# Kernel optimization log

Measured on AMD Instinct MI355X. Metric: run time of the kernel, lower is better.

Reference implementation:

```python
import jax, jax.numpy as jnp
import numpy as np

NU, NF, E, FIN, H = 50000, 25000, 500000, 128, 128
NEG_SLOPE_ATT = 0.2   # PyG GATConv default negative_slope
NEG_SLOPE_MLP = 0.01  # nn.LeakyReLU default
BN_EPS = 1e-5


def setup_inputs() -> dict:
    key = jax.random.key(0)
    ks = iter(jax.random.split(key, 64))

    def rn(shape, scale=0.05):
        return jax.random.normal(next(ks), shape, dtype=jnp.float32) * scale

    inp = {
        "x_user": jax.random.normal(next(ks), (NU, FIN), dtype=jnp.float32),
        "x_food": jax.random.normal(next(ks), (NF, FIN), dtype=jnp.float32),
        "uf_src": jax.random.randint(next(ks), (E,), 0, NU),
        "uf_dst": jax.random.randint(next(ks), (E,), 0, NF),
        "fu_src": jax.random.randint(next(ks), (E,), 0, NF),
        "fu_dst": jax.random.randint(next(ks), (E,), 0, NU),
        "he_user": jax.random.randint(next(ks), (E,), 0, NU),
        "he_food": jax.random.randint(next(ks), (E,), 0, NF),
        "batch_health_scores": jax.random.uniform(next(ks), (E,), dtype=jnp.float32),
    }
    # GATConv params per layer (1,2) per edge type (uf: user->food, fu: food->user)
    for L, fin in ((1, FIN), (2, H)):
        for et in ("uf", "fu"):
            inp[f"w{L}_{et}_src"] = rn((fin, H))
            inp[f"w{L}_{et}_dst"] = rn((fin, H))
            inp[f"a{L}_{et}_src"] = rn((H,))
            inp[f"a{L}_{et}_dst"] = rn((H,))
            inp[f"b{L}_{et}"] = jnp.zeros((H,), jnp.float32)
    # BatchNorm per layer per node type
    for L in (1, 2):
        for nt in ("user", "food"):
            inp[f"bn{L}_{nt}_g"] = jnp.ones((H,), jnp.float32)
            inp[f"bn{L}_{nt}_b"] = jnp.zeros((H,), jnp.float32)
    # health preference MLP: Linear(H, H//2) -> LeakyReLU -> Linear(H//2, 1) -> Tanh
    inp["hw1"] = rn((H, H // 2)); inp["hb1"] = jnp.zeros((H // 2,), jnp.float32)
    inp["hw2"] = rn((H // 2, 1)); inp["hb2"] = jnp.zeros((1,), jnp.float32)
    return inp


def _gat(x_src, x_dst, src, dst, w_s, w_d, a_s, a_d, b, n_dst):
    """PyG GATConv, heads=1, no self loops, eval (no attention dropout)."""
    hs = x_src @ w_s                      # [Ns, H]
    hd = x_dst @ w_d                      # [Nd, H]
    asn = hs @ a_s                        # per-src-node scalar
    adn = hd @ a_d                        # per-dst-node scalar
    e = jax.nn.leaky_relu(asn[src] + adn[dst], NEG_SLOPE_ATT)  # [E]
    m = jax.ops.segment_max(e, dst, num_segments=n_dst)
    m = jnp.where(jnp.isfinite(m), m, 0.0)
    ee = jnp.exp(e - m[dst])
    den = jax.ops.segment_sum(ee, dst, num_segments=n_dst)
    alpha = ee / (den[dst] + 1e-16)
    out = jax.ops.segment_sum(alpha[:, None] * hs[src], dst, num_segments=n_dst)
    return out + b


def _bn_elu(x, g, b):
    mu = x.mean(0)
    var = x.var(0)  # biased var, as torch BN uses for normalization
    return jax.nn.elu((x - mu) * jax.lax.rsqrt(var + BN_EPS) * g + b)


def reference(x_user, x_food, uf_src, uf_dst, fu_src, fu_dst, he_user, he_food,
              batch_health_scores,
              w1_uf_src, w1_uf_dst, a1_uf_src, a1_uf_dst, b1_uf,
              w1_fu_src, w1_fu_dst, a1_fu_src, a1_fu_dst, b1_fu,
              w2_uf_src, w2_uf_dst, a2_uf_src, a2_uf_dst, b2_uf,
              w2_fu_src, w2_fu_dst, a2_fu_src, a2_fu_dst, b2_fu,
              bn1_user_g, bn1_user_b, bn1_food_g, bn1_food_b,
              bn2_user_g, bn2_user_b, bn2_food_g, bn2_food_b,
              hw1, hb1, hw2, hb2):
    # ---- layer 1 (HeteroConv, sum aggr; each node type has one incoming edge type)
    xf = _gat(x_user, x_food, uf_src, uf_dst, w1_uf_src, w1_uf_dst, a1_uf_src, a1_uf_dst, b1_uf, NF)
    xu = _gat(x_food, x_user, fu_src, fu_dst, w1_fu_src, w1_fu_dst, a1_fu_src, a1_fu_dst, b1_fu, NU)
    xu = _bn_elu(xu, bn1_user_g, bn1_user_b)
    xf = _bn_elu(xf, bn1_food_g, bn1_food_b)
    # ---- layer 2
    xf2 = _gat(xu, xf, uf_src, uf_dst, w2_uf_src, w2_uf_dst, a2_uf_src, a2_uf_dst, b2_uf, NF)
    xu2 = _gat(xf, xu, fu_src, fu_dst, w2_fu_src, w2_fu_dst, a2_fu_src, a2_fu_dst, b2_fu, NU)
    xu2 = _bn_elu(xu2, bn2_user_g, bn2_user_b)
    xf2 = _bn_elu(xf2, bn2_food_g, bn2_food_b)
    # ---- health-score scatter_add update
    h = jax.nn.leaky_relu(xu2 @ hw1 + hb1, NEG_SLOPE_MLP)
    prefs = jnp.tanh(h @ hw2 + hb2)                      # [NU, 1]
    adjusted = prefs[he_user, 0] * batch_health_scores   # [E]
    # expand+scatter_add over rows == broadcast segment_sum of the per-edge scalar
    s = jax.ops.segment_sum(adjusted, he_food, num_segments=NF)  # [NF]
    xf2 = xf2 + 0.1 * s[:, None]
    return (xu2, xf2, prefs)
```

## Files before the change

kernel.cpp:

```cpp
#include <hip/hip_runtime.h>
#include <cstddef>

#define NU_ 50000
#define NF_ 25000
#define E_  500000
#define CAPF_ 96
#define CAPU_ 48

typedef __attribute__((ext_vector_type(8))) short short8v;
typedef __attribute__((ext_vector_type(4))) float float4v;

constexpr int LDR = 136;

static __device__ __forceinline__ ushort f2bf(float f) {
    uint u = __float_as_uint(f);
    uint r = (u + 0x7fffu + ((u >> 16) & 1u)) >> 16;
    return (ushort)r;
}
static __device__ __forceinline__ float bf2f(ushort u) {
    return __uint_as_float(((uint)u) << 16);
}

struct PPArgs {
    const int* uf_src; const int* uf_dst;
    const int* fu_src; const int* fu_dst;
    int* deg_f; int* deg_u;
    ushort* buck_f; ushort* buck_u;
    const float* xu; const float* xf;
    ushort* bu; ushort* bfo;
    const float* W[5];  ushort* T[5];
    const float* waW[8]; const float* waA[8];
    float* vall;
};

__global__ __launch_bounds__(256) void preprocess(PPArgs A) {
    const int EB  = (E_ + 255) / 256;
    const int nbA = NU_ * 32 / 256;
    const int nbB = NF_ * 32 / 256;
    const int nbC = 4 * 64 + 32;
    int b = blockIdx.x, t = threadIdx.x;
    if (b < 2 * EB) {
        const int *src, *dst; int *deg; ushort* buck; int cap, e;
        if (b < EB) { src = A.uf_src; dst = A.uf_dst; deg = A.deg_f; buck = A.buck_f; cap = CAPF_; e = b * 256 + t; }
        else        { src = A.fu_src; dst = A.fu_dst; deg = A.deg_u; buck = A.buck_u; cap = CAPU_; e = (b - EB) * 256 + t; }
        if (e < E_) {
            int d = dst[e];
            int r = atomicAdd(&deg[d], 1);
            if (r < cap) buck[d * cap + r] = (ushort)src[e];
        }
        return;
    }
    b -= 2 * EB;
    if (b < nbA) {
        int i = b * 256 + t;
        float4 v = ((const float4*)A.xu)[i];
        ushort4 o; o.x = f2bf(v.x); o.y = f2bf(v.y); o.z = f2bf(v.z); o.w = f2bf(v.w);
        ((ushort4*)A.bu)[i] = o;
    } else if (b < nbA + nbB) {
        int i = (b - nbA) * 256 + t;
        float4 v = ((const float4*)A.xf)[i];
        ushort4 o; o.x = f2bf(v.x); o.y = f2bf(v.y); o.z = f2bf(v.z); o.w = f2bf(v.w);
        ((ushort4*)A.bfo)[i] = o;
    } else if (b < nbA + nbB + nbC) {
        int cb = b - nbA - nbB;
        int m, wb, sh;
        if (cb < 256) { m = cb >> 6; wb = cb & 63; sh = 7; }
        else          { m = 4; wb = cb - 256; sh = 6; }
        int idx = wb * 256 + t;
        int k = idx >> sh, c = idx & ((1 << sh) - 1);
        A.T[m][c * 128 + k] = f2bf(A.W[m][idx]);
    } else {
        int db = b - nbA - nbB - nbC;
        int row = db * 4 + (t >> 6);
        int m = row >> 7, k = row & 127, lane = t & 63;
        float2 w = ((const float2*)(A.waW[m] + k * 128))[lane];
        float2 av = ((const float2*)A.waA[m])[lane];
        float s = w.x * av.x + w.y * av.y;
        #pragma unroll
        for (int o = 32; o; o >>= 1) s += __shfl_xor(s, o);
        if (lane == 0) A.vall[row] = s;
    }
}

static __device__ __forceinline__ void gemm_tile(const ushort* __restrict__ Xb,
                                                 const ushort* __restrict__ Wt,
                                                 ushort* __restrict__ C, int N, int row0,
                                                 const float* __restrict__ va, const float* __restrict__ vb,
                                                 float* __restrict__ oa, float* __restrict__ ob,
                                                 short* Xs, short* Ws) {
    const int t = threadIdx.x;
    for (int i = t; i < 128 * 16; i += 256) {
        int r = i >> 4, c8 = (i & 15) << 3;
        short8v v = {};
        if (row0 + r < N) v = *(const short8v*)(Xb + (size_t)(row0 + r) * 128 + c8);
        *(short8v*)(&Xs[r * LDR + c8]) = v;
    }
    for (int i = t; i < 128 * 16; i += 256) {
        int r = i >> 4, c8 = (i & 15) << 3;
        *(short8v*)(&Ws[r * LDR + c8]) = *(const short8v*)(Wt + r * 128 + c8);
    }
    __syncthreads();

    const int w = t >> 6, l = t & 63;
    const int m0 = (w & 1) * 64;
    const int n0 = (w >> 1) * 64;
    const int frow = l & 15;
    const int koff = (l >> 4) << 3;

    float4v acc[4][4];
    #pragma unroll
    for (int m = 0; m < 4; ++m)
        #pragma unroll
        for (int n = 0; n < 4; ++n) acc[m][n] = (float4v)0.f;

    #pragma unroll
    for (int ks = 0; ks < 4; ++ks) {
        const int k0 = ks * 32 + koff;
        short8v a[4], b[4];
        #pragma unroll
        for (int m = 0; m < 4; ++m)
            a[m] = *(const short8v*)(&Xs[(m0 + m * 16 + frow) * LDR + k0]);
        #pragma unroll
        for (int n = 0; n < 4; ++n)
            b[n] = *(const short8v*)(&Ws[(n0 + n * 16 + frow) * LDR + k0]);
        #pragma unroll
        for (int m = 0; m < 4; ++m)
            #pragma unroll
            for (int n = 0; n < 4; ++n)
                acc[m][n] = __builtin_amdgcn_mfma_f32_16x16x32_bf16(a[m], b[n], acc[m][n], 0, 0, 0);
    }

    const int crow = (l >> 4) << 2;
    const int ccol = l & 15;
    #pragma unroll
    for (int m = 0; m < 4; ++m) {
        #pragma unroll
        for (int r4 = 0; r4 < 4; ++r4) {
            int grow = row0 + m0 + m * 16 + crow + r4;
            if (grow < N) {
                #pragma unroll
                for (int n = 0; n < 4; ++n)
                    C[(size_t)grow * 128 + n0 + n * 16 + ccol] = f2bf(acc[m][n][r4]);
            }
        }
    }

    float2 va2 = ((const float2*)va)[l];
    float2 vb2 = ((const float2*)vb)[l];
    for (int rr = 0; rr < 32; ++rr) {
        int r = w * 32 + rr;
        ushort2 xv = *(const ushort2*)(&Xs[r * LDR + l * 2]);
        float fx = bf2f(xv.x), fy = bf2f(xv.y);
        float s1 = fx * va2.x + fy * va2.y;
        float s2 = fx * vb2.x + fy * vb2.y;
        #pragma unroll
        for (int o = 32; o; o >>= 1) { s1 += __shfl_xor(s1, o); s2 += __shfl_xor(s2, o); }
        int grow = row0 + r;
        if (l == 0 && grow < N) { oa[grow] = s1; ob[grow] = s2; }
    }
}

__global__ __launch_bounds__(256) void gemm_both(
        const ushort* __restrict__ Xu, const ushort* __restrict__ Wtu, ushort* __restrict__ Cu,
        const float* __restrict__ vau, const float* __restrict__ vbu,
        float* __restrict__ oau, float* __restrict__ obu,
        const ushort* __restrict__ Xf, const ushort* __restrict__ Wtf, ushort* __restrict__ Cf,
        const float* __restrict__ vaf, const float* __restrict__ vbf,
        float* __restrict__ oaf, float* __restrict__ obf) {
    __shared__ short Xs[128 * LDR];
    __shared__ short Ws[128 * LDR];
    const int GU = (NU_ + 127) / 128;
    if ((int)blockIdx.x < GU)
        gemm_tile(Xu, Wtu, Cu, NU_, blockIdx.x * 128, vau, vbu, oau, obu, Xs, Ws);
    else
        gemm_tile(Xf, Wtf, Cf, NF_, (blockIdx.x - GU) * 128, vaf, vbf, oaf, obf, Xs, Ws);
}

__global__ __launch_bounds__(256) void gat_agg_both(
        const int* __restrict__ deg_f, const ushort* __restrict__ buck_f,
        const float* __restrict__ asn_u, const float* __restrict__ adn_f,
        const ushort* __restrict__ hs_u, ushort* __restrict__ out_f,
        const int* __restrict__ deg_u, const ushort* __restrict__ buck_u,
        const float* __restrict__ asn_f, const float* __restrict__ adn_u,
        const ushort* __restrict__ hs_f, ushort* __restrict__ out_u) {
    const int NBAF = (NF_ + 3) / 4;
    int blk = blockIdx.x;
    const int* deg; const ushort* buck; const float *asn, *adn; const ushort* hs; ushort* out; int Nd, d, cap;
    if (blk < NBAF) {
        deg = deg_f; buck = buck_f; asn = asn_u; adn = adn_f; hs = hs_u; out = out_f;
        Nd = NF_; cap = CAPF_; d = blk * 4 + (threadIdx.x >> 6);
    } else {
        deg = deg_u; buck = buck_u; asn = asn_f; adn = adn_u; hs = hs_f; out = out_u;
        Nd = NU_; cap = CAPU_; d = (blk - NBAF) * 4 + (threadIdx.x >> 6);
    }
    int lane = threadIdx.x & 63;
    if (d >= Nd) return;
    const int beg = d * cap;
    const int end = beg + min(deg[d], cap);
    const float ad = adn[d];
    const int qw = lane >> 4, l16 = lane & 15;
    float acc[8] = {0.f, 0.f, 0.f, 0.f, 0.f, 0.f, 0.f, 0.f};
    float den = 0.f;
    for (int base = beg; base < end; base += 64) {
        int e = base + lane;
        int s = 0; float ev = 0.f;
        if (e < end) {
            s = buck[e];
            float v = asn[s] + ad;
            v = v > 0.f ? v : 0.2f * v;
            ev = __expf(v);
        }
        float r = ev;
        #pragma unroll
        for (int o = 32; o; o >>= 1) r += __shfl_xor(r, o);
        den += r;
        int cnt4 = (min(64, end - base) + 3) & ~3;
        for (int j = 0; j < cnt4; j += 8) {
            int jj = j + qw;
            float ev0 = __shfl(ev, jj);
            int   sj0 = __shfl(s, jj);
            short8v h0 = *(const short8v*)(hs + (size_t)sj0 * 128 + l16 * 8);
            if (j + 4 < cnt4) {
                float ev1 = __shfl(ev, jj + 4);
                int   sj1 = __shfl(s, jj + 4);
                short8v h1 = *(const short8v*)(hs + (size_t)sj1 * 128 + l16 * 8);
                #pragma unroll
                for (int k = 0; k < 8; ++k)
                    acc[k] += ev0 * bf2f((ushort)h0[k]) + ev1 * bf2f((ushort)h1[k]);
            } else {
                #pragma unroll
                for (int k = 0; k < 8; ++k)
                    acc[k] += ev0 * bf2f((ushort)h0[k]);
            }
        }
    }
    #pragma unroll
    for (int k = 0; k < 8; ++k) {
        acc[k] += __shfl_xor(acc[k], 16);
        acc[k] += __shfl_xor(acc[k], 32);
    }
    if (qw == 0) {
        float inv = 1.f / (den + 1e-16f);
        short8v o;
        #pragma unroll
        for (int k = 0; k < 8; ++k) o[k] = (short)f2bf(acc[k] * inv);
        *(short8v*)(out + (size_t)d * 128 + l16 * 8) = o;
    }
}

__global__ __launch_bounds__(256) void bn_stats2b(const ushort* __restrict__ x1, float* __restrict__ stat1,
                                                  int N1, int B1,
                                                  const ushort* __restrict__ x2, float* __restrict__ stat2,
                                                  int N2, int B2) {
    const ushort* x; float* stat; int N, b, nb;
    if ((int)blockIdx.x < B1) { x = x1; stat = stat1; N = N1; b = blockIdx.x; nb = B1; }
    else { x = x2; stat = stat2; N = N2; b = blockIdx.x - B1; nb = B2; }
    const int t = threadIdx.x;
    const int rg = t >> 4;
    const int c16 = t & 15;
    float s[8] = {0,0,0,0,0,0,0,0}, q[8] = {0,0,0,0,0,0,0,0};
    for (int r = b * 16 + rg; r < N; r += nb * 16) {
        short8v v = *(const short8v*)(x + (size_t)r * 128 + c16 * 8);
        #pragma unroll
        for (int k = 0; k < 8; ++k) {
            float f = bf2f((ushort)v[k]);
            s[k] += f; q[k] += f * f;
        }
    }
    #pragma unroll
    for (int k = 0; k < 8; ++k) {
        s[k] += __shfl_xor(s[k], 16); q[k] += __shfl_xor(q[k], 16);
        s[k] += __shfl_xor(s[k], 32); q[k] += __shfl_xor(q[k], 32);
    }
    __shared__ float rs[4][128], rq[4][128];
    const int w = t >> 6, l = t & 63;
    if (l < 16) {
        #pragma unroll
        for (int k = 0; k < 8; ++k) {
            rs[w][l * 8 + k] = s[k];
            rq[w][l * 8 + k] = q[k];
        }
    }
    __syncthreads();
    if (t < 128) {
        atomicAdd(&stat[t],       rs[0][t] + rs[1][t] + rs[2][t] + rs[3][t]);
        atomicAdd(&stat[128 + t], rq[0][t] + rq[1][t] + rq[2][t] + rq[3][t]);
    }
}

static __device__ __forceinline__ void bn_scale_shift(const float* __restrict__ stat,
                                                      const float* __restrict__ g,
                                                      const float* __restrict__ b,
                                                      float invN, int c0,
                                                      float* sc, float* sh) {
    #pragma unroll
    for (int k = 0; k < 8; ++k) {
        int c = c0 + k;
        float mu  = stat[c] * invN;
        float var = stat[128 + c] * invN - mu * mu;
        float s = g[c] * rsqrtf(var + 1e-5f);
        sc[k] = s;
        sh[k] = b[c] - mu * s;
    }
}

__global__ void bn_apply2b(const ushort* __restrict__ x1, const float* __restrict__ stat1,
                           const float* __restrict__ g1, const float* __restrict__ b1, float invN1,
                           float* __restrict__ xo1, ushort* __restrict__ xb1, int N1,
                           const ushort* __restrict__ x2, const float* __restrict__ stat2,
                           const float* __restrict__ g2, const float* __restrict__ b2, float invN2,
                           float* __restrict__ xo2, ushort* __restrict__ xb2, int N2) {
    int i = blockIdx.x * 256 + threadIdx.x;
    const ushort* x; const float *stat, *g, *b; float invN; float* xo; ushort* xb;
    if (i < N1 * 16) { x = x1; stat = stat1; g = g1; b = b1; invN = invN1; xo = xo1; xb = xb1; }
    else {
        i -= N1 * 16;
        if (i >= N2 * 16) return;
        x = x2; stat = stat2; g = g2; b = b2; invN = invN2; xo = xo2; xb = xb2;
    }
    int c16 = i & 15;
    short8v v = *(const short8v*)(x + (size_t)i * 8);
    float sc[8], sh[8];
    bn_scale_shift(stat, g, b, invN, c16 * 8, sc, sh);
    float o[8];
    #pragma unroll
    for (int k = 0; k < 8; ++k) {
        float f = bf2f((ushort)v[k]) * sc[k] + sh[k];
        o[k] = f > 0.f ? f : __expf(f) - 1.f;
    }
    if (xo) {
        *(float4*)(xo + (size_t)i * 8)     = make_float4(o[0], o[1], o[2], o[3]);
        *(float4*)(xo + (size_t)i * 8 + 4) = make_float4(o[4], o[5], o[6], o[7]);
    }
    if (xb) {
        short8v u;
        #pragma unroll
        for (int k = 0; k < 8; ++k) u[k] = (short)f2bf(o[k]);
        *(short8v*)(xb + (size_t)i * 8) = u;
    }
}

__global__ void bn_apply1b(const ushort* __restrict__ x, const float* __restrict__ stat,
                           const float* __restrict__ g, const float* __restrict__ b, float invN,
                           float* __restrict__ xo, ushort* __restrict__ xb, int N,
                           const float* __restrict__ health) {
    int i = blockIdx.x * 256 + threadIdx.x;
    if (i >= N * 16) return;
    int c16 = i & 15;
    short8v v = *(const short8v*)(x + (size_t)i * 8);
    float sc[8], sh[8];
    bn_scale_shift(stat, g, b, invN, c16 * 8, sc, sh);
    float hv = health ? 0.1f * health[i >> 4] : 0.f;
    float o[8];
    #pragma unroll
    for (int k = 0; k < 8; ++k) {
        float f = bf2f((ushort)v[k]) * sc[k] + sh[k];
        o[k] = (f > 0.f ? f : __expf(f) - 1.f) + hv;
    }
    if (xo) {
        *(float4*)(xo + (size_t)i * 8)     = make_float4(o[0], o[1], o[2], o[3]);
        *(float4*)(xo + (size_t)i * 8 + 4) = make_float4(o[4], o[5], o[6], o[7]);
    }
    if (xb) {
        short8v u;
        #pragma unroll
        for (int k = 0; k < 8; ++k) u[k] = (short)f2bf(o[k]);
        *(short8v*)(xb + (size_t)i * 8) = u;
    }
}

__global__ __launch_bounds__(256) void mlp_mfma(const ushort* __restrict__ Xb,
                                                const ushort* __restrict__ Wt,
                                                const float* __restrict__ hb1,
                                                const float* __restrict__ hw2,
                                                const float* __restrict__ hb2,
                                                float* __restrict__ prefs, int N) {
    __shared__ short Xs[128 * LDR];
    __shared__ short Ws[64 * LDR];
    const int t = threadIdx.x;
    const int row0 = blockIdx.x * 128;

    for (int i = t; i < 128 * 16; i += 256) {
        int r = i >> 4, c8 = (i & 15) << 3;
        short8v v = {};
        if (row0 + r < N) v = *(const short8v*)(Xb + (size_t)(row0 + r) * 128 + c8);
        *(short8v*)(&Xs[r * LDR + c8]) = v;
    }
    for (int i = t; i < 64 * 16; i += 256) {
        int r = i >> 4, c8 = (i & 15) << 3;
        *(short8v*)(&Ws[r * LDR + c8]) = *(const short8v*)(Wt + r * 128 + c8);
    }
    __syncthreads();

    const int w = t >> 6, l = t & 63;
    const int m0 = w * 32;
    const int frow = l & 15;
    const int koff = (l >> 4) << 3;

    float4v acc[2][4];
    #pragma unroll
    for (int m = 0; m < 2; ++m)
        #pragma unroll
        for (int n = 0; n < 4; ++n) acc[m][n] = (float4v)0.f;

    #pragma unroll
    for (int ks = 0; ks < 4; ++ks) {
        const int k0 = ks * 32 + koff;
        short8v a[2], b[4];
        #pragma unroll
        for (int m = 0; m < 2; ++m)
            a[m] = *(const short8v*)(&Xs[(m0 + m * 16 + frow) * LDR + k0]);
        #pragma unroll
        for (int n = 0; n < 4; ++n)
            b[n] = *(const short8v*)(&Ws[(n * 16 + frow) * LDR + k0]);
        #pragma unroll
        for (int m = 0; m < 2; ++m)
            #pragma unroll
            for (int n = 0; n < 4; ++n)
                acc[m][n] = __builtin_amdgcn_mfma_f32_16x16x32_bf16(a[m], b[n], acc[m][n], 0, 0, 0);
    }

    float hb1v[4], hw2v[4];
    #pragma unroll
    for (int n = 0; n < 4; ++n) {
        int col = n * 16 + (l & 15);
        hb1v[n] = hb1[col];
        hw2v[n] = hw2[col];
    }
    const float hb2v = hb2[0];
    #pragma unroll
    for (int m = 0; m < 2; ++m) {
        #pragma unroll
        for (int r4 = 0; r4 < 4; ++r4) {
            float p = 0.f;
            #pragma unroll
            for (int n = 0; n < 4; ++n) {
                float v = acc[m][n][r4] + hb1v[n];
                v = v > 0.f ? v : 0.01f * v;
                p += v * hw2v[n];
            }
            p += __shfl_xor(p, 1);
            p += __shfl_xor(p, 2);
            p += __shfl_xor(p, 4);
            p += __shfl_xor(p, 8);
            int grow = row0 + m0 + m * 16 + ((l >> 4) << 2) + r4;
            if ((l & 15) == 0 && grow < N) prefs[grow] = tanhf(p + hb2v);
        }
    }
}

__global__ void health_scatter(const int* __restrict__ hu, const int* __restrict__ hf,
                               const float* __restrict__ score, const float* __restrict__ prefs,
                               float* __restrict__ s, int E) {
    int e = blockIdx.x * 256 + threadIdx.x;
    if (e >= E) return;
    atomicAdd(&s[hf[e]], prefs[hu[e]] * score[e]);
}

extern "C" void kernel_launch(void* const* d_in, const int* in_sizes, int n_in,
                              void* d_out, int out_size, void* d_ws, size_t ws_size,
                              hipStream_t stream) {
    const float* x_user = (const float*)d_in[0];
    const float* x_food = (const float*)d_in[1];
    const int* uf_src = (const int*)d_in[2];
    const int* uf_dst = (const int*)d_in[3];
    const int* fu_src = (const int*)d_in[4];
    const int* fu_dst = (const int*)d_in[5];
    const int* he_user = (const int*)d_in[6];
    const int* he_food = (const int*)d_in[7];
    const float* scores = (const float*)d_in[8];
    const float* bn1_user_g = (const float*)d_in[29];
    const float* bn1_user_b = (const float*)d_in[30];
    const float* bn1_food_g = (const float*)d_in[31];
    const float* bn1_food_b = (const float*)d_in[32];
    const float* bn2_user_g = (const float*)d_in[33];
    const float* bn2_user_b = (const float*)d_in[34];
    const float* bn2_food_g = (const float*)d_in[35];
    const float* bn2_food_b = (const float*)d_in[36];
    const float* hw1 = (const float*)d_in[37];
    const float* hb1 = (const float*)d_in[38];
    const float* hw2 = (const float*)d_in[39];
    const float* hb2 = (const float*)d_in[40];

    float* outp  = (float*)d_out;
    float* xu2   = outp;
    float* xf2   = outp + (size_t)NU_ * 128;
    float* prefs = xf2 + (size_t)NF_ * 128;

    float* ws = (float*)d_ws;
    ushort* hs_u = (ushort*)ws;
    ushort* hs_f = hs_u + (size_t)NU_ * 128;
    float* base1 = ws + (size_t)(NU_ + NF_) * 64;
    ushort* xu1b = (ushort*)base1;
    ushort* xf1b = xu1b + (size_t)NU_ * 128;
    float* base2 = base1 + (size_t)(NU_ + NF_) * 64;
    ushort* xu2b = (ushort*)base2;
    ushort* xf2b = xu2b + (size_t)NU_ * 128;
    float* base3 = base2 + (size_t)(NU_ + NF_) * 64;
    float* asn_u = base3;
    float* adn_u = asn_u + NU_;
    float* asn_f = adn_u + NU_;
    float* adn_f = asn_f + NF_;
    float* stat4 = adn_f + NF_;
    float* sbuf  = stat4 + 1024;
    int*   deg_f = (int*)(sbuf + NF_);
    int*   deg_u = deg_f + NF_;
    ushort* buck_f = (ushort*)(deg_u + NU_);
    ushort* buck_u = buck_f + (size_t)NF_ * CAPF_;
    ushort* wt0  = buck_u + (size_t)NU_ * CAPU_;
    ushort* wt1  = wt0 + 16384;
    ushort* wt2  = wt1 + 16384;
    ushort* wt3  = wt2 + 16384;
    ushort* hw1t = wt3 + 16384;
    float* vall  = (float*)(hw1t + 8192);

    const size_t zero_elems = 1024 + NF_ + NF_ + NU_;
    hipMemsetAsync(stat4, 0, zero_elems * sizeof(float), stream);

    const int EB = (E_ + 255) / 256;
    PPArgs pp;
    pp.uf_src = uf_src; pp.uf_dst = uf_dst;
    pp.fu_src = fu_src; pp.fu_dst = fu_dst;
    pp.deg_f = deg_f; pp.deg_u = deg_u;
    pp.buck_f = buck_f; pp.buck_u = buck_u;
    pp.xu = x_user; pp.xf = x_food; pp.bu = xu2b; pp.bfo = xf2b;
    pp.W[0] = (const float*)d_in[9];  pp.T[0] = wt0;
    pp.W[1] = (const float*)d_in[14]; pp.T[1] = wt1;
    pp.W[2] = (const float*)d_in[19]; pp.T[2] = wt2;
    pp.W[3] = (const float*)d_in[24]; pp.T[3] = wt3;
    pp.W[4] = hw1;                    pp.T[4] = hw1t;
    pp.waW[0] = (const float*)d_in[9];  pp.waA[0] = (const float*)d_in[11];
    pp.waW[1] = (const float*)d_in[10]; pp.waA[1] = (const float*)d_in[12];
    pp.waW[2] = (const float*)d_in[14]; pp.waA[2] = (const float*)d_in[16];
    pp.waW[3] = (const float*)d_in[15]; pp.waA[3] = (const float*)d_in[17];
    pp.waW[4] = (const float*)d_in[19]; pp.waA[4] = (const float*)d_in[21];
    pp.waW[5] = (const float*)d_in[20]; pp.waA[5] = (const float*)d_in[22];
    pp.waW[6] = (const float*)d_in[24]; pp.waA[6] = (const float*)d_in[26];
    pp.waW[7] = (const float*)d_in[25]; pp.waA[7] = (const float*)d_in[27];
    pp.vall = vall;
    const int PPB = 2 * EB + NU_ * 32 / 256 + NF_ * 32 / 256 + 288 + 256;
    preprocess<<<PPB, 256, 0, stream>>>(pp);

    const int GB  = (NU_ + 127) / 128 + (NF_ + 127) / 128;
    const int AGB = (NF_ + 3) / 4 + (NU_ + 3) / 4;
    const int APB = ((NU_ + NF_) * 16 + 255) / 256;
    const float invNU = 1.0f / NU_, invNF = 1.0f / NF_;

    gemm_both<<<GB, 256, 0, stream>>>(
        xu2b, wt0, hs_u, vall + 0,   vall + 384, asn_u, adn_u,
        xf2b, wt1, hs_f, vall + 256, vall + 128, asn_f, adn_f);
    gat_agg_both<<<AGB, 256, 0, stream>>>(deg_f, buck_f, asn_u, adn_f, hs_u, xf1b,
                                          deg_u, buck_u, asn_f, adn_u, hs_f, xu1b);
    bn_stats2b<<<768, 256, 0, stream>>>(xu1b, stat4 + 0, NU_, 512, xf1b, stat4 + 256, NF_, 256);
    bn_apply2b<<<APB, 256, 0, stream>>>(
        xu1b, stat4 + 0,   bn1_user_g, bn1_user_b, invNU, (float*)nullptr, xu1b, NU_,
        xf1b, stat4 + 256, bn1_food_g, bn1_food_b, invNF, (float*)nullptr, xf1b, NF_);

    gemm_both<<<GB, 256, 0, stream>>>(
        xu1b, wt2, hs_u, vall + 512, vall + 896, asn_u, adn_u,
        xf1b, wt3, hs_f, vall + 768, vall + 640, asn_f, adn_f);
    gat_agg_both<<<AGB, 256, 0, stream>>>(deg_f, buck_f, asn_u, adn_f, hs_u, xf2b,
                                          deg_u, buck_u, asn_f, adn_u, hs_f, xu2b);
    bn_stats2b<<<768, 256, 0, stream>>>(xu2b, stat4 + 512, NU_, 512, xf2b, stat4 + 768, NF_, 256);
    bn_apply1b<<<(NU_ * 16 + 255) / 256, 256, 0, stream>>>(
        xu2b, stat4 + 512, bn2_user_g, bn2_user_b, invNU, xu2, xu2b, NU_, (const float*)nullptr);
    mlp_mfma<<<(NU_ + 127) / 128, 256, 0, stream>>>(xu2b, hw1t, hb1, hw2, hb2, prefs, NU_);
    health_scatter<<<EB, 256, 0, stream>>>(he_user, he_food, scores, prefs, sbuf, E_);
    bn_apply1b<<<(NF_ * 16 + 255) / 256, 256, 0, stream>>>(
        xf2b, stat4 + 768, bn2_food_g, bn2_food_b, invNF, xf2, (ushort*)nullptr, NF_, sbuf);
}
```

Baseline: 336.5 us.

## Partition edge bucketing by destination range and split attention matvecs into own kernel

The edge-bucketing phase now launches eight times as many blocks. Each block handles only destinations in one eighth of the node range, so the atomics and bucket writes of concurrently running blocks land in a narrower address range. The per-node attention dot products move out of the GEMM epilogue into a separate matvec kernel that reads the bf16 inputs again. This shortens the serial shuffle-reduction tail in the GEMM, but costs extra reads of the edge indices, an extra pass over the node features and two more launches.

```diff
diff --git a/kernel.cpp b/kernel.cpp
--- a/kernel.cpp
+++ b/kernel.cpp
@@ -35,22 +35,28 @@
 
 __global__ __launch_bounds__(256) void preprocess(PPArgs A) {
     const int EB  = (E_ + 255) / 256;
+    const int FBLK = 8 * EB;
     const int nbA = NU_ * 32 / 256;
     const int nbB = NF_ * 32 / 256;
     const int nbC = 4 * 64 + 32;
     int b = blockIdx.x, t = threadIdx.x;
-    if (b < 2 * EB) {
-        const int *src, *dst; int *deg; ushort* buck; int cap, e;
-        if (b < EB) { src = A.uf_src; dst = A.uf_dst; deg = A.deg_f; buck = A.buck_f; cap = CAPF_; e = b * 256 + t; }
-        else        { src = A.fu_src; dst = A.fu_dst; deg = A.deg_u; buck = A.buck_u; cap = CAPU_; e = (b - EB) * 256 + t; }
+    if (b < 2 * FBLK) {
+        const int *src, *dst; int *deg; ushort* buck; int cap, Nd;
+        int cb = b;
+        if (cb < FBLK) { src = A.uf_src; dst = A.uf_dst; deg = A.deg_f; buck = A.buck_f; cap = CAPF_; Nd = NF_; }
+        else           { src = A.fu_src; dst = A.fu_dst; deg = A.deg_u; buck = A.buck_u; cap = CAPU_; Nd = NU_; cb -= FBLK; }
+        int p = cb & 7;
+        int e = (cb >> 3) * 256 + t;
         if (e < E_) {
             int d = dst[e];
-            int r = atomicAdd(&deg[d], 1);
-            if (r < cap) buck[d * cap + r] = (ushort)src[e];
+            if ((d * 8) / Nd == p) {
+                int r = atomicAdd(&deg[d], 1);
+                if (r < cap) buck[d * cap + r] = (ushort)src[e];
+            }
         }
         return;
     }
-    b -= 2 * EB;
+    b -= 2 * FBLK;
     if (b < nbA) {
         int i = b * 256 + t;
         float4 v = ((const float4*)A.xu)[i];
@@ -85,8 +91,6 @@
 static __device__ __forceinline__ void gemm_tile(const ushort* __restrict__ Xb,
                                                  const ushort* __restrict__ Wt,
                                                  ushort* __restrict__ C, int N, int row0,
-                                                 const float* __restrict__ va, const float* __restrict__ vb,
-                                                 float* __restrict__ oa, float* __restrict__ ob,
                                                  short* Xs, short* Ws) {
     const int t = threadIdx.x;
     for (int i = t; i < 128 * 16; i += 256) {
@@ -144,36 +148,44 @@
             }
         }
     }
-
-    float2 va2 = ((const float2*)va)[l];
-    float2 vb2 = ((const float2*)vb)[l];
-    for (int rr = 0; rr < 32; ++rr) {
-        int r = w * 32 + rr;
-        ushort2 xv = *(const ushort2*)(&Xs[r * LDR + l * 2]);
-        float fx = bf2f(xv.x), fy = bf2f(xv.y);
-        float s1 = fx * va2.x + fy * va2.y;
-        float s2 = fx * vb2.x + fy * vb2.y;
-        #pragma unroll
-        for (int o = 32; o; o >>= 1) { s1 += __shfl_xor(s1, o); s2 += __shfl_xor(s2, o); }
-        int grow = row0 + r;
-        if (l == 0 && grow < N) { oa[grow] = s1; ob[grow] = s2; }
-    }
-}
-
-__global__ __launch_bounds__(256) void gemm_both(
-        const ushort* __restrict__ Xu, const ushort* __restrict__ Wtu, ushort* __restrict__ Cu,
-        const float* __restrict__ vau, const float* __restrict__ vbu,
-        float* __restrict__ oau, float* __restrict__ obu,
-        const ushort* __restrict__ Xf, const ushort* __restrict__ Wtf, ushort* __restrict__ Cf,
-        const float* __restrict__ vaf, const float* __restrict__ vbf,
-        float* __restrict__ oaf, float* __restrict__ obf) {
+}
+
+__global__ __launch_bounds__(256) void gemm_both(const ushort* __restrict__ Xu, const ushort* __restrict__ Wtu,
+                                                 ushort* __restrict__ Cu,
+                                                 const ushort* __restrict__ Xf, const ushort* __restrict__ Wtf,
+                                                 ushort* __restrict__ Cf) {
     __shared__ short Xs[128 * LDR];
     __shared__ short Ws[128 * LDR];
     const int GU = (NU_ + 127) / 128;
     if ((int)blockIdx.x < GU)
-        gemm_tile(Xu, Wtu, Cu, NU_, blockIdx.x * 128, vau, vbu, oau, obu, Xs, Ws);
+        gemm_tile(Xu, Wtu, Cu, NU_, blockIdx.x * 128, Xs, Ws);
     else
-        gemm_tile(Xf, Wtf, Cf, NF_, (blockIdx.x - GU) * 128, vaf, vbf, oaf, obf, Xs, Ws);
+        gemm_tile(Xf, Wtf, Cf, NF_, (blockIdx.x - GU) * 128, Xs, Ws);
+}
+
+__global__ __launch_bounds__(256) void matvec4(const ushort* __restrict__ bu, const ushort* __restrict__ bfo,
+                                               const float* __restrict__ v_asn_u, const float* __restrict__ v_adn_u,
+                                               const float* __restrict__ v_adn_f, const float* __restrict__ v_asn_f,
+                                               float* __restrict__ asn_u, float* __restrict__ adn_u,
+                                               float* __restrict__ adn_f, float* __restrict__ asn_f) {
+    int row = blockIdx.x * 4 + (threadIdx.x >> 6);
+    int lane = threadIdx.x & 63;
+    const ushort* X; const float *va, *vb; float *oa, *ob; int r;
+    if (row < NU_) { X = bu; va = v_asn_u; vb = v_adn_u; oa = asn_u; ob = adn_u; r = row; }
+    else {
+        r = row - NU_;
+        if (r >= NF_) return;
+        X = bfo; va = v_adn_f; vb = v_asn_f; oa = adn_f; ob = asn_f;
+    }
+    ushort2 x = ((const ushort2*)(X + (size_t)r * 128))[lane];
+    float2 va2 = ((const float2*)va)[lane];
+    float2 vb2 = ((const float2*)vb)[lane];
+    float fx = bf2f(x.x), fy = bf2f(x.y);
+    float s1 = fx * va2.x + fy * va2.y;
+    float s2 = fx * vb2.x + fy * vb2.y;
+    #pragma unroll
+    for (int o = 32; o; o >>= 1) { s1 += __shfl_xor(s1, o); s2 += __shfl_xor(s2, o); }
+    if (lane == 0) { oa[r] = s1; ob[r] = s2; }
 }
 
 __global__ __launch_bounds__(256) void gat_agg_both(
@@ -518,6 +530,7 @@
     hipMemsetAsync(stat4, 0, zero_elems * sizeof(float), stream);
 
     const int EB = (E_ + 255) / 256;
+    const int FBLK = 8 * EB;
     PPArgs pp;
     pp.uf_src = uf_src; pp.uf_dst = uf_dst;
     pp.fu_src = fu_src; pp.fu_dst = fu_dst;
@@ -538,17 +551,18 @@
     pp.waW[6] = (const float*)d_in[24]; pp.waA[6] = (const float*)d_in[26];
     pp.waW[7] = (const float*)d_in[25]; pp.waA[7] = (const float*)d_in[27];
     pp.vall = vall;
-    const int PPB = 2 * EB + NU_ * 32 / 256 + NF_ * 32 / 256 + 288 + 256;
+    const int PPB = 2 * FBLK + NU_ * 32 / 256 + NF_ * 32 / 256 + 288 + 256;
     preprocess<<<PPB, 256, 0, stream>>>(pp);
 
     const int GB  = (NU_ + 127) / 128 + (NF_ + 127) / 128;
+    const int MVB = (NU_ + NF_ + 3) / 4;
     const int AGB = (NF_ + 3) / 4 + (NU_ + 3) / 4;
     const int APB = ((NU_ + NF_) * 16 + 255) / 256;
     const float invNU = 1.0f / NU_, invNF = 1.0f / NF_;
 
-    gemm_both<<<GB, 256, 0, stream>>>(
-        xu2b, wt0, hs_u, vall + 0,   vall + 384, asn_u, adn_u,
-        xf2b, wt1, hs_f, vall + 256, vall + 128, asn_f, adn_f);
+    gemm_both<<<GB, 256, 0, stream>>>(xu2b, wt0, hs_u, xf2b, wt1, hs_f);
+    matvec4<<<MVB, 256, 0, stream>>>(xu2b, xf2b, vall + 0, vall + 384, vall + 128, vall + 256,
+                                     asn_u, adn_u, adn_f, asn_f);
     gat_agg_both<<<AGB, 256, 0, stream>>>(deg_f, buck_f, asn_u, adn_f, hs_u, xf1b,
                                           deg_u, buck_u, asn_f, adn_u, hs_f, xu1b);
     bn_stats2b<<<768, 256, 0, stream>>>(xu1b, stat4 + 0, NU_, 512, xf1b, stat4 + 256, NF_, 256);
@@ -556,9 +570,9 @@
         xu1b, stat4 + 0,   bn1_user_g, bn1_user_b, invNU, (float*)nullptr, xu1b, NU_,
         xf1b, stat4 + 256, bn1_food_g, bn1_food_b, invNF, (float*)nullptr, xf1b, NF_);
 
-    gemm_both<<<GB, 256, 0, stream>>>(
-        xu1b, wt2, hs_u, vall + 512, vall + 896, asn_u, adn_u,
-        xf1b, wt3, hs_f, vall + 768, vall + 640, asn_f, adn_f);
+    gemm_both<<<GB, 256, 0, stream>>>(xu1b, wt2, hs_u, xf1b, wt3, hs_f);
+    matvec4<<<MVB, 256, 0, stream>>>(xu1b, xf1b, vall + 512, vall + 896, vall + 640, vall + 768,
+                                     asn_u, adn_u, adn_f, asn_f);
     gat_agg_both<<<AGB, 256, 0, stream>>>(deg_f, buck_f, asn_u, adn_f, hs_u, xf2b,
                                           deg_u, buck_u, asn_f, adn_u, hs_f, xu2b);
     bn_stats2b<<<768, 256, 0, stream>>>(xu2b, stat4 + 512, NU_, 512, xf2b, stat4 + 768, NF_, 256);
```

After: 313.1 us (median of 2 runs). 7.0% less time.
